# Kernel optimization log

Measured on AMD Instinct MI355X. Metric: run time of the kernel, lower is better.

Reference implementation:

```python
import jax, jax.numpy as jnp
import numpy as np

N, G, H = 500_000, 25_000, 256


def setup_inputs() -> dict:
    key = jax.random.key(0)
    ks = jax.random.split(key, 8)
    node = jax.random.normal(ks[0], (N, H), dtype=jnp.float32)
    super_node = jax.random.normal(ks[1], (G, H), dtype=jnp.float32)
    segment_ids = jnp.sort(jax.random.randint(ks[2], (N,), 0, G, dtype=jnp.int32))
    s = 0.05
    return {
        "node": node,
        "super_node": super_node,
        "segment_ids": segment_ids,
        "w_align": jax.random.normal(ks[3], (2 * H, 1), jnp.float32) * s,
        "b_align": jnp.zeros((1,), jnp.float32),
        "w_attend": jax.random.normal(ks[4], (H, H), jnp.float32) * s,
        "b_attend": jnp.zeros((H,), jnp.float32),
        "w_ih": jax.random.normal(ks[5], (H, 3 * H), jnp.float32) * s,
        "w_hh": jax.random.normal(ks[6], (H, 3 * H), jnp.float32) * s,
        "b_ih": jnp.zeros((3 * H,), jnp.float32),
        "b_hh": jnp.zeros((3 * H,), jnp.float32),
    }


def reference(node, super_node, segment_ids, w_align, b_align, w_attend,
              b_attend, w_ih, w_hh, b_ih, b_hh):
    g = super_node.shape[0]
    h = node.shape[1]
    # super_node = F.leaky_relu(super_node)
    s = jax.nn.leaky_relu(super_node)  # slope 0.01 (torch default)
    # cal_alignment(cat([node, broadcast_nodes(super)])) == node@Wn + (s@Ws)[seg]
    wn, ws = w_align[:h], w_align[h:]
    score = jax.nn.leaky_relu(node @ wn + (s @ ws)[segment_ids] + b_align)  # [N,1]
    # softmax_nodes: segment-wise stable softmax
    m = jax.ops.segment_max(score, segment_ids, num_segments=g)
    w = jnp.exp(score - m[segment_ids])
    denom = jax.ops.segment_sum(w, segment_ids, num_segments=g)
    attn = w / denom[segment_ids]  # [N,1]
    # attend (dropout=0, eval)
    hidden = node @ w_attend + b_attend  # [N,H]
    # sum_nodes weighted by attention, then ELU
    ctx = jax.nn.elu(jax.ops.segment_sum(attn * hidden, segment_ids, num_segments=g))  # [G,H]
    # GRUCell(ctx, s) per torch semantics
    gi = ctx @ w_ih + b_ih
    gh = s @ w_hh + b_hh
    ir, iz, inn = jnp.split(gi, 3, axis=-1)
    hr, hz, hn = jnp.split(gh, 3, axis=-1)
    r = jax.nn.sigmoid(ir + hr)
    z = jax.nn.sigmoid(iz + hz)
    n = jnp.tanh(inn + r * hn)
    new_h = (1.0 - z) * n + z * s
    return jax.nn.relu(new_h), attn
```

## Files before the change

### kernel.cpp

```cpp
#include <hip/hip_runtime.h>
#include <math.h>

#define N_NODES 500000
#define G_SEG   25000
#define H_DIM   256
#define SPB     4

typedef __attribute__((ext_vector_type(4))) float f32x4;
typedef __attribute__((ext_vector_type(8))) short bf16x8;

__device__ __forceinline__ float leaky(float x){ return x > 0.f ? x : 0.01f * x; }

__device__ __forceinline__ ushort f2bf(float f){
  unsigned u = __float_as_uint(f);
  u += 0x7FFFu + ((u >> 16) & 1u);
  return (ushort)(u >> 16);
}

__global__ __launch_bounds__(256) void kPrep(
    const float* __restrict__ sn, const float* __restrict__ w_align,
    const int* __restrict__ seg, const float* __restrict__ w_att,
    const float* __restrict__ w_ih, const float* __restrict__ w_hh,
    float* __restrict__ s_buf, float* __restrict__ sws,
    int* __restrict__ starts, ushort* __restrict__ Bp,
    ushort* __restrict__ Bp6)
{
  int b = blockIdx.x, t = threadIdx.x;

  {
    float v = sn[b * H_DIM + t];
    float sv = leaky(v);
    s_buf[b * H_DIM + t] = sv;
    float p = sv * w_align[H_DIM + t];
    #pragma unroll
    for (int d = 1; d < 64; d <<= 1) p += __shfl_xor(p, d);
    __shared__ float red[4];
    int wid = t >> 6, lane = t & 63;
    if (lane == 0) red[wid] = p;
    __syncthreads();
    if (t == 0) sws[b] = red[0] + red[1] + red[2] + red[3];
  }

  if (b < 1954) {
    int i = b * 256 + t;
    if (i < N_NODES) {
      int s = seg[i];
      int prev = (i == 0) ? -1 : seg[i - 1];
      for (int g = prev + 1; g <= s; g++) starts[g] = i;
      if (i == N_NODES - 1)
        for (int g = s + 1; g <= G_SEG; g++) starts[g] = N_NODES;
    }
  }
  else if (b >= 2000 && b < 2256) {
    int kk = b - 2000;
    Bp[(((kk >> 3) << 8) + t) * 8 + (kk & 7)] = f2bf(w_att[kk * H_DIM + t]);
  }
  else if (b >= 2256 && b < 2768) {
    int kk = b - 2256;
    #pragma unroll
    for (int gate = 0; gate < 4; gate++) {
      float v;
      if (gate == 0)      v = (kk < 256) ? w_ih[kk * 768 + t]        : w_hh[(kk - 256) * 768 + t];
      else if (gate == 1) v = (kk < 256) ? w_ih[kk * 768 + 256 + t]  : w_hh[(kk - 256) * 768 + 256 + t];
      else if (gate == 2) v = (kk < 256) ? w_ih[kk * 768 + 512 + t]  : 0.f;
      else                v = (kk < 256) ? 0.f                       : w_hh[(kk - 256) * 768 + 512 + t];
      int n = (gate << 8) + t;
      Bp6[(((kk >> 3) << 10) + n) * 8 + (kk & 7)] = f2bf(v);
    }
  }
}

__global__ __launch_bounds__(256) void kF_score_softmax_agg(
    const float* __restrict__ node, const int* __restrict__ starts,
    const float* __restrict__ w_align, const float* __restrict__ b_align,
    const float* __restrict__ sws,
    float* __restrict__ attn_out, float* __restrict__ agg,
    float* __restrict__ bscale)
{
  __shared__ int st_s[SPB + 1];
  const int tid = threadIdx.x;
  const int g0 = blockIdx.x * SPB;
  if (tid <= SPB) st_s[tid] = starts[g0 + tid];
  __syncthreads();

  const int wv = tid >> 6, lane = tid & 63;
  const float4 wvec = ((const float4*)w_align)[lane];
  const float b0 = b_align[0];

  const int g  = g0 + wv;
  const int st = st_s[wv], en = st_s[wv + 1];
  const float swsg = sws[g];

  float m = -3.4e38f, sum = 0.f;
  f32x4 pacc = {0.f, 0.f, 0.f, 0.f};

  int r = st;
  for (; r + 3 < en; r += 4) {
    f32x4 a0 = ((const f32x4*)node)[(size_t)(r    ) * 64 + lane];
    f32x4 a1 = ((const f32x4*)node)[(size_t)(r + 1) * 64 + lane];
    f32x4 a2 = ((const f32x4*)node)[(size_t)(r + 2) * 64 + lane];
    f32x4 a3 = ((const f32x4*)node)[(size_t)(r + 3) * 64 + lane];
    float d0 = a0[0]*wvec.x + a0[1]*wvec.y + a0[2]*wvec.z + a0[3]*wvec.w;
    float d1 = a1[0]*wvec.x + a1[1]*wvec.y + a1[2]*wvec.z + a1[3]*wvec.w;
    float d2 = a2[0]*wvec.x + a2[1]*wvec.y + a2[2]*wvec.z + a2[3]*wvec.w;
    float d3 = a3[0]*wvec.x + a3[1]*wvec.y + a3[2]*wvec.z + a3[3]*wvec.w;

    float k01 = (lane & 1) ? d1 : d0;
    float s01 = (lane & 1) ? d0 : d1;
    k01 += __shfl_xor(s01, 1);
    float k23 = (lane & 1) ? d3 : d2;
    float s23 = (lane & 1) ? d2 : d3;
    k23 += __shfl_xor(s23, 1);
    float x  = (lane & 2) ? k23 : k01;
    float xs = (lane & 2) ? k01 : k23;
    x += __shfl_xor(xs, 2);
    x += __shfl_xor(x, 4);
    x += __shfl_xor(x, 8);
    x += __shfl_xor(x, 16);
    x += __shfl_xor(x, 32);

    float sc = leaky(x + swsg + b0);
    if (lane < 4) attn_out[r + lane] = sc;

    float bm = fmaxf(sc, __shfl_xor(sc, 1));
    bm = fmaxf(bm, __shfl_xor(bm, 2));
    if (bm > m) {
      float scale = __expf(m - bm);
      sum *= scale; pacc *= scale; m = bm;
    }
    float p = __expf(sc - m);
    float p0 = __shfl(p, 0);
    float p1 = __shfl(p, 1);
    float p2 = __shfl(p, 2);
    float p3 = __shfl(p, 3);
    sum += (p0 + p1) + (p2 + p3);
    pacc += p0 * a0 + p1 * a1;
    pacc += p2 * a2 + p3 * a3;
  }
  for (; r < en; r++) {
    f32x4 a = ((const f32x4*)node)[(size_t)r * 64 + lane];
    float d = a[0]*wvec.x + a[1]*wvec.y + a[2]*wvec.z + a[3]*wvec.w;
    #pragma unroll
    for (int s2 = 1; s2 < 64; s2 <<= 1) d += __shfl_xor(d, s2);
    float sc = leaky(d + swsg + b0);
    if (lane == 0) attn_out[r] = sc;
    if (sc <= m) {
      float p = __expf(sc - m);
      sum += p;
      pacc += p * a;
    } else {
      float scale = __expf(m - sc);
      sum = sum * scale + 1.f;
      pacc = pacc * scale + a;
      m = sc;
    }
  }

  float invD = (sum > 0.f) ? 1.f / sum : 0.f;
  ((f32x4*)(agg + (size_t)g * H_DIM))[lane] = pacc * invD;
  if (lane == 0) bscale[g] = (sum > 0.f) ? 1.f : 0.f;
  for (int rr = st + lane; rr < en; rr += 64)
    attn_out[rr] = __expf(attn_out[rr] - m) * invD;
}

__global__ __launch_bounds__(256, 2) void k5b_ctx(
    const float* __restrict__ agg, const ushort* __restrict__ Bp,
    const float* __restrict__ b_att, const float* __restrict__ bscale,
    float* __restrict__ ctx)
{
  __shared__ __align__(16) ushort A_lds[128 * 256];

  const int tid  = threadIdx.x;
  const int row0 = blockIdx.x * 128;

  #pragma unroll
  for (int i = 0; i < 16; i++) {
    int v = tid + i * 256;
    int r = v >> 5;
    int s = v & 31;
    int grow = row0 + r;
    f32x4 x0 = {0.f, 0.f, 0.f, 0.f}, x1 = {0.f, 0.f, 0.f, 0.f};
    if (grow < G_SEG) {
      const f32x4* p = (const f32x4*)(agg + (size_t)grow * H_DIM) + s * 2;
      x0 = p[0]; x1 = p[1];
    }
    bf16x8 t;
    t[0] = (short)f2bf(x0[0]); t[1] = (short)f2bf(x0[1]);
    t[2] = (short)f2bf(x0[2]); t[3] = (short)f2bf(x0[3]);
    t[4] = (short)f2bf(x1[0]); t[5] = (short)f2bf(x1[1]);
    t[6] = (short)f2bf(x1[2]); t[7] = (short)f2bf(x1[3]);
    *(bf16x8*)&A_lds[r * 256 + ((s ^ (r & 7)) * 8)] = t;
  }
  __syncthreads();

  const int wv  = tid >> 6;
  const int l   = tid & 63;
  const int l15 = l & 15, lq = l >> 4, l7 = l & 7;
  const int colbase = wv * 64 + l15;

  f32x4 acc[8][4];
  #pragma unroll
  for (int mf = 0; mf < 8; mf++)
    #pragma unroll
    for (int nf = 0; nf < 4; nf++)
      acc[mf][nf] = (f32x4){0.f, 0.f, 0.f, 0.f};

  for (int ks = 0; ks < 8; ks++) {
    int c = ks * 4 + lq;
    bf16x8 b[4];
    #pragma unroll
    for (int nf = 0; nf < 4; nf++)
      b[nf] = *(const bf16x8*)&Bp[(((c << 8) + colbase + nf * 16)) * 8];
    bf16x8 a[8];
    #pragma unroll
    for (int mf = 0; mf < 8; mf++)
      a[mf] = *(const bf16x8*)&A_lds[(mf * 16 + l15) * 256 + ((c ^ l7) * 8)];
    #pragma unroll
    for (int mf = 0; mf < 8; mf++)
      #pragma unroll
      for (int nf = 0; nf < 4; nf++)
        acc[mf][nf] = __builtin_amdgcn_mfma_f32_16x16x32_bf16(
            a[mf], b[nf], acc[mf][nf], 0, 0, 0);
  }

  float bias[4];
  #pragma unroll
  for (int nf = 0; nf < 4; nf++) bias[nf] = b_att[colbase + nf * 16];

  #pragma unroll
  for (int mf = 0; mf < 8; mf++) {
    #pragma unroll
    for (int r = 0; r < 4; r++) {
      int grow = row0 + mf * 16 + lq * 4 + r;
      if (grow < G_SEG) {
        float bsc = bscale[grow];
        #pragma unroll
        for (int nf = 0; nf < 4; nf++)
          ctx[(size_t)grow * H_DIM + colbase + nf * 16] =
              acc[mf][nf][r] + bias[nf] * bsc;
      }
    }
  }
}

__global__ __launch_bounds__(512, 2) void k6_mfma(
    const float* __restrict__ ctxbuf, const float* __restrict__ s_buf,
    const ushort* __restrict__ Bp6,
    const float* __restrict__ b_ih, const float* __restrict__ b_hh,
    float* __restrict__ out0)
{
  __shared__ __align__(16) ushort A_lds[64 * 512];

  const int tid  = threadIdx.x;
  const int row0 = blockIdx.x * 64;

  #pragma unroll
  for (int i = 0; i < 8; i++) {
    int v = tid + i * 512;
    int r = v >> 6;
    int s = v & 63;
    int g = row0 + r;
    f32x4 x0 = {0.f, 0.f, 0.f, 0.f}, x1 = {0.f, 0.f, 0.f, 0.f};
    if (g < G_SEG) {
      const f32x4* p = (s < 32)
          ? (const f32x4*)(ctxbuf + (size_t)g * H_DIM) + s * 2
          : (const f32x4*)(s_buf + (size_t)g * H_DIM) + (s - 32) * 2;
      x0 = p[0]; x1 = p[1];
      if (s < 32) {
        #pragma unroll
        for (int e = 0; e < 4; e++) {
          x0[e] = x0[e] > 0.f ? x0[e] : (__expf(x0[e]) - 1.f);
          x1[e] = x1[e] > 0.f ? x1[e] : (__expf(x1[e]) - 1.f);
        }
      }
    }
    bf16x8 t;
    t[0] = (short)f2bf(x0[0]); t[1] = (short)f2bf(x0[1]);
    t[2] = (short)f2bf(x0[2]); t[3] = (short)f2bf(x0[3]);
    t[4] = (short)f2bf(x1[0]); t[5] = (short)f2bf(x1[1]);
    t[6] = (short)f2bf(x1[2]); t[7] = (short)f2bf(x1[3]);
    *(bf16x8*)&A_lds[r * 512 + ((s ^ (r & 7)) * 8)] = t;
  }
  __syncthreads();

  const int wv  = tid >> 6;
  const int rh  = (wv >> 2) * 32;
  const int cw  = (wv & 3) << 6;
  const int l   = tid & 63;
  const int l15 = l & 15, lq = l >> 4, l7 = l & 7;

  f32x4 acc[4][2][4];
  #pragma unroll
  for (int gt = 0; gt < 4; gt++)
    #pragma unroll
    for (int mf = 0; mf < 2; mf++)
      #pragma unroll
      for (int nf = 0; nf < 4; nf++)
        acc[gt][mf][nf] = (f32x4){0.f, 0.f, 0.f, 0.f};

  for (int ks = 0; ks < 16; ks++) {
    int c = ks * 4 + lq;
    bf16x8 a[2];
    #pragma unroll
    for (int mf = 0; mf < 2; mf++)
      a[mf] = *(const bf16x8*)&A_lds[(rh + mf * 16 + l15) * 512 + ((c ^ l7) * 8)];
    #pragma unroll
    for (int gt = 0; gt < 4; gt++) {
      if (gt == 2 && ks >= 8) continue;
      if (gt == 3 && ks < 8) continue;
      #pragma unroll
      for (int nf = 0; nf < 4; nf++) {
        int n = (gt << 8) + cw + nf * 16 + l15;
        bf16x8 b = *(const bf16x8*)&Bp6[(((c << 10) + n)) * 8];
        acc[gt][0][nf] = __builtin_amdgcn_mfma_f32_16x16x32_bf16(
            a[0], b, acc[gt][0][nf], 0, 0, 0);
        acc[gt][1][nf] = __builtin_amdgcn_mfma_f32_16x16x32_bf16(
            a[1], b, acc[gt][1][nf], 0, 0, 0);
      }
    }
  }

  #pragma unroll
  for (int nf = 0; nf < 4; nf++) {
    int cc = cw + nf * 16 + l15;
    float bir = b_ih[cc] + b_hh[cc];
    float biz = b_ih[256 + cc] + b_hh[256 + cc];
    float bin_ = b_ih[512 + cc];
    float bhn  = b_hh[512 + cc];
    #pragma unroll
    for (int mf = 0; mf < 2; mf++) {
      #pragma unroll
      for (int rr = 0; rr < 4; rr++) {
        int grow = row0 + rh + mf * 16 + lq * 4 + rr;
        if (grow < G_SEG) {
          float v0 = acc[0][mf][nf][rr];
          float v1 = acc[1][mf][nf][rr];
          float v2 = acc[2][mf][nf][rr];
          float v3 = acc[3][mf][nf][rr];
          float r_ = 1.f / (1.f + __expf(-(v0 + bir)));
          float z_ = 1.f / (1.f + __expf(-(v1 + biz)));
          float n_ = tanhf(v2 + bin_ + r_ * (v3 + bhn));
          float sv = s_buf[(size_t)grow * H_DIM + cc];
          float nh = (1.f - z_) * n_ + z_ * sv;
          out0[(size_t)grow * H_DIM + cc] = nh > 0.f ? nh : 0.f;
        }
      }
    }
  }
}

extern "C" void kernel_launch(void* const* d_in, const int* in_sizes, int n_in,
                              void* d_out, int out_size, void* d_ws, size_t ws_size,
                              hipStream_t stream)
{
  (void)in_sizes; (void)n_in; (void)out_size; (void)ws_size;
  const float* node       = (const float*)d_in[0];
  const float* super_node = (const float*)d_in[1];
  const int*   seg        = (const int*)d_in[2];
  const float* w_align    = (const float*)d_in[3];
  const float* b_align    = (const float*)d_in[4];
  const float* w_att      = (const float*)d_in[5];
  const float* b_att      = (const float*)d_in[6];
  const float* w_ih       = (const float*)d_in[7];
  const float* w_hh       = (const float*)d_in[8];
  const float* b_ih       = (const float*)d_in[9];
  const float* b_hh       = (const float*)d_in[10];

  float* out0     = (float*)d_out;
  float* attn_out = (float*)d_out + (size_t)G_SEG * H_DIM;

  float* ws     = (float*)d_ws;
  float* s_buf  = ws;
  float* sws    = ws + 6400000;
  float* agg    = ws + 6425000;
  ushort* Bp    = (ushort*)(ws + 12825000);
  ushort* Bp6   = (ushort*)(ws + 12860000);
  float* bscale = ws + 13125000;
  int*   starts = (int*)(ws + 13150000);
  float* ctx    = ws + 13200000;

  kPrep<<<G_SEG, 256, 0, stream>>>(super_node, w_align, seg, w_att, w_ih, w_hh,
                                   s_buf, sws, starts, Bp, Bp6);
  kF_score_softmax_agg<<<G_SEG / SPB, 256, 0, stream>>>(
      node, starts, w_align, b_align, sws, attn_out, agg, bscale);
  k5b_ctx<<<(G_SEG + 127) / 128, 256, 0, stream>>>(agg, Bp, b_att, bscale, ctx);
  k6_mfma<<<(G_SEG + 63) / 64, 512, 0, stream>>>(ctx, s_buf, Bp6, b_ih, b_hh, out0);
}
```

Measured before the change: 263.4 us.

## Vectorize prep, unroll score loop by 8, emit ELU'd bf16 ctx

kPrep now handles four super-nodes per block, one wavefront each, using float4 loads and a wave-only reduction instead of an LDS reduction and barrier. The grid shrinks to G/4 blocks. The segment-softmax aggregation loop is unrolled from 4 to 8 rows per iteration to keep more node loads in flight. k5b now applies ELU and stores ctx as bf16, which halves the intermediate traffic and removes the conversion work from k6. The costs are higher register pressure in the unrolled loop and bf16 rounding of ctx one step earlier, which matches what k6 already did.

```diff
diff --git a/kernel.cpp b/kernel.cpp
--- a/kernel.cpp
+++ b/kernel.cpp
@@ -26,19 +26,19 @@
     ushort* __restrict__ Bp6)
 {
   int b = blockIdx.x, t = threadIdx.x;
+  int wv = t >> 6, lane = t & 63;
 
   {
-    float v = sn[b * H_DIM + t];
-    float sv = leaky(v);
-    s_buf[b * H_DIM + t] = sv;
-    float p = sv * w_align[H_DIM + t];
+    int g = b * 4 + wv;
+    f32x4 sv = ((const f32x4*)(sn + (size_t)g * H_DIM))[lane];
+    f32x4 wa = ((const f32x4*)(w_align + H_DIM))[lane];
+    #pragma unroll
+    for (int e = 0; e < 4; e++) sv[e] = leaky(sv[e]);
+    ((f32x4*)(s_buf + (size_t)g * H_DIM))[lane] = sv;
+    float p = sv[0]*wa[0] + sv[1]*wa[1] + sv[2]*wa[2] + sv[3]*wa[3];
     #pragma unroll
     for (int d = 1; d < 64; d <<= 1) p += __shfl_xor(p, d);
-    __shared__ float red[4];
-    int wid = t >> 6, lane = t & 63;
-    if (lane == 0) red[wid] = p;
-    __syncthreads();
-    if (t == 0) sws[b] = red[0] + red[1] + red[2] + red[3];
+    if (lane == 0) sws[g] = p;
   }
 
   if (b < 1954) {
@@ -95,47 +95,62 @@
   f32x4 pacc = {0.f, 0.f, 0.f, 0.f};
 
   int r = st;
-  for (; r + 3 < en; r += 4) {
+  for (; r + 7 < en; r += 8) {
     f32x4 a0 = ((const f32x4*)node)[(size_t)(r    ) * 64 + lane];
     f32x4 a1 = ((const f32x4*)node)[(size_t)(r + 1) * 64 + lane];
     f32x4 a2 = ((const f32x4*)node)[(size_t)(r + 2) * 64 + lane];
     f32x4 a3 = ((const f32x4*)node)[(size_t)(r + 3) * 64 + lane];
+    f32x4 a4 = ((const f32x4*)node)[(size_t)(r + 4) * 64 + lane];
+    f32x4 a5 = ((const f32x4*)node)[(size_t)(r + 5) * 64 + lane];
+    f32x4 a6 = ((const f32x4*)node)[(size_t)(r + 6) * 64 + lane];
+    f32x4 a7 = ((const f32x4*)node)[(size_t)(r + 7) * 64 + lane];
     float d0 = a0[0]*wvec.x + a0[1]*wvec.y + a0[2]*wvec.z + a0[3]*wvec.w;
     float d1 = a1[0]*wvec.x + a1[1]*wvec.y + a1[2]*wvec.z + a1[3]*wvec.w;
     float d2 = a2[0]*wvec.x + a2[1]*wvec.y + a2[2]*wvec.z + a2[3]*wvec.w;
     float d3 = a3[0]*wvec.x + a3[1]*wvec.y + a3[2]*wvec.z + a3[3]*wvec.w;
-
-    float k01 = (lane & 1) ? d1 : d0;
-    float s01 = (lane & 1) ? d0 : d1;
+    float d4 = a4[0]*wvec.x + a4[1]*wvec.y + a4[2]*wvec.z + a4[3]*wvec.w;
+    float d5 = a5[0]*wvec.x + a5[1]*wvec.y + a5[2]*wvec.z + a5[3]*wvec.w;
+    float d6 = a6[0]*wvec.x + a6[1]*wvec.y + a6[2]*wvec.z + a6[3]*wvec.w;
+    float d7 = a7[0]*wvec.x + a7[1]*wvec.y + a7[2]*wvec.z + a7[3]*wvec.w;
+
+    float k01 = (lane & 1) ? d1 : d0, s01 = (lane & 1) ? d0 : d1;
     k01 += __shfl_xor(s01, 1);
-    float k23 = (lane & 1) ? d3 : d2;
-    float s23 = (lane & 1) ? d2 : d3;
+    float k23 = (lane & 1) ? d3 : d2, s23 = (lane & 1) ? d2 : d3;
     k23 += __shfl_xor(s23, 1);
-    float x  = (lane & 2) ? k23 : k01;
-    float xs = (lane & 2) ? k01 : k23;
-    x += __shfl_xor(xs, 2);
-    x += __shfl_xor(x, 4);
+    float k45 = (lane & 1) ? d5 : d4, s45 = (lane & 1) ? d4 : d5;
+    k45 += __shfl_xor(s45, 1);
+    float k67 = (lane & 1) ? d7 : d6, s67 = (lane & 1) ? d6 : d7;
+    k67 += __shfl_xor(s67, 1);
+    float xa = (lane & 2) ? k23 : k01, sa = (lane & 2) ? k01 : k23;
+    xa += __shfl_xor(sa, 2);
+    float xb = (lane & 2) ? k67 : k45, sb = (lane & 2) ? k45 : k67;
+    xb += __shfl_xor(sb, 2);
+    float x = (lane & 4) ? xb : xa, sx = (lane & 4) ? xa : xb;
+    x += __shfl_xor(sx, 4);
     x += __shfl_xor(x, 8);
     x += __shfl_xor(x, 16);
     x += __shfl_xor(x, 32);
 
     float sc = leaky(x + swsg + b0);
-    if (lane < 4) attn_out[r + lane] = sc;
+    if (lane < 8) attn_out[r + lane] = sc;
 
     float bm = fmaxf(sc, __shfl_xor(sc, 1));
     bm = fmaxf(bm, __shfl_xor(bm, 2));
+    bm = fmaxf(bm, __shfl_xor(bm, 4));
     if (bm > m) {
       float scale = __expf(m - bm);
       sum *= scale; pacc *= scale; m = bm;
     }
     float p = __expf(sc - m);
-    float p0 = __shfl(p, 0);
-    float p1 = __shfl(p, 1);
-    float p2 = __shfl(p, 2);
-    float p3 = __shfl(p, 3);
-    sum += (p0 + p1) + (p2 + p3);
+    float p0 = __shfl(p, 0), p1 = __shfl(p, 1);
+    float p2 = __shfl(p, 2), p3 = __shfl(p, 3);
+    float p4 = __shfl(p, 4), p5 = __shfl(p, 5);
+    float p6 = __shfl(p, 6), p7 = __shfl(p, 7);
+    sum += ((p0 + p1) + (p2 + p3)) + ((p4 + p5) + (p6 + p7));
     pacc += p0 * a0 + p1 * a1;
     pacc += p2 * a2 + p3 * a3;
+    pacc += p4 * a4 + p5 * a5;
+    pacc += p6 * a6 + p7 * a7;
   }
   for (; r < en; r++) {
     f32x4 a = ((const f32x4*)node)[(size_t)r * 64 + lane];
@@ -166,7 +181,7 @@
 __global__ __launch_bounds__(256, 2) void k5b_ctx(
     const float* __restrict__ agg, const ushort* __restrict__ Bp,
     const float* __restrict__ b_att, const float* __restrict__ bscale,
-    float* __restrict__ ctx)
+    ushort* __restrict__ ctx_bf16)
 {
   __shared__ __align__(16) ushort A_lds[128 * 256];
 
@@ -235,16 +250,18 @@
       if (grow < G_SEG) {
         float bsc = bscale[grow];
         #pragma unroll
-        for (int nf = 0; nf < 4; nf++)
-          ctx[(size_t)grow * H_DIM + colbase + nf * 16] =
-              acc[mf][nf][r] + bias[nf] * bsc;
+        for (int nf = 0; nf < 4; nf++) {
+          float val = acc[mf][nf][r] + bias[nf] * bsc;
+          val = val > 0.f ? val : (__expf(val) - 1.f);
+          ctx_bf16[(size_t)grow * H_DIM + colbase + nf * 16] = f2bf(val);
+        }
       }
     }
   }
 }
 
 __global__ __launch_bounds__(512, 2) void k6_mfma(
-    const float* __restrict__ ctxbuf, const float* __restrict__ s_buf,
+    const ushort* __restrict__ ctx_bf16, const float* __restrict__ s_buf,
     const ushort* __restrict__ Bp6,
     const float* __restrict__ b_ih, const float* __restrict__ b_hh,
     float* __restrict__ out0)
@@ -260,25 +277,19 @@
     int r = v >> 6;
     int s = v & 63;
     int g = row0 + r;
-    f32x4 x0 = {0.f, 0.f, 0.f, 0.f}, x1 = {0.f, 0.f, 0.f, 0.f};
+    bf16x8 t = {0,0,0,0,0,0,0,0};
     if (g < G_SEG) {
-      const f32x4* p = (s < 32)
-          ? (const f32x4*)(ctxbuf + (size_t)g * H_DIM) + s * 2
-          : (const f32x4*)(s_buf + (size_t)g * H_DIM) + (s - 32) * 2;
-      x0 = p[0]; x1 = p[1];
       if (s < 32) {
-        #pragma unroll
-        for (int e = 0; e < 4; e++) {
-          x0[e] = x0[e] > 0.f ? x0[e] : (__expf(x0[e]) - 1.f);
-          x1[e] = x1[e] > 0.f ? x1[e] : (__expf(x1[e]) - 1.f);
-        }
+        t = ((const bf16x8*)(ctx_bf16 + (size_t)g * H_DIM))[s];
+      } else {
+        const f32x4* p = (const f32x4*)(s_buf + (size_t)g * H_DIM) + (s - 32) * 2;
+        f32x4 y0 = p[0], y1 = p[1];
+        t[0] = (short)f2bf(y0[0]); t[1] = (short)f2bf(y0[1]);
+        t[2] = (short)f2bf(y0[2]); t[3] = (short)f2bf(y0[3]);
+        t[4] = (short)f2bf(y1[0]); t[5] = (short)f2bf(y1[1]);
+        t[6] = (short)f2bf(y1[2]); t[7] = (short)f2bf(y1[3]);
       }
     }
-    bf16x8 t;
-    t[0] = (short)f2bf(x0[0]); t[1] = (short)f2bf(x0[1]);
-    t[2] = (short)f2bf(x0[2]); t[3] = (short)f2bf(x0[3]);
-    t[4] = (short)f2bf(x1[0]); t[5] = (short)f2bf(x1[1]);
-    t[6] = (short)f2bf(x1[2]); t[7] = (short)f2bf(x1[3]);
     *(bf16x8*)&A_lds[r * 512 + ((s ^ (r & 7)) * 8)] = t;
   }
   __syncthreads();
@@ -377,12 +388,12 @@
   ushort* Bp6   = (ushort*)(ws + 12860000);
   float* bscale = ws + 13125000;
   int*   starts = (int*)(ws + 13150000);
-  float* ctx    = ws + 13200000;
-
-  kPrep<<<G_SEG, 256, 0, stream>>>(super_node, w_align, seg, w_att, w_ih, w_hh,
-                                   s_buf, sws, starts, Bp, Bp6);
+  ushort* ctx_bf16 = (ushort*)(ws + 13200000);
+
+  kPrep<<<G_SEG / 4, 256, 0, stream>>>(super_node, w_align, seg, w_att, w_ih, w_hh,
+                                       s_buf, sws, starts, Bp, Bp6);
   kF_score_softmax_agg<<<G_SEG / SPB, 256, 0, stream>>>(
       node, starts, w_align, b_align, sws, attn_out, agg, bscale);
-  k5b_ctx<<<(G_SEG + 127) / 128, 256, 0, stream>>>(agg, Bp, b_att, bscale, ctx);
-  k6_mfma<<<(G_SEG + 63) / 64, 512, 0, stream>>>(ctx, s_buf, Bp6, b_ih, b_hh, out0);
-}
+  k5b_ctx<<<(G_SEG + 127) / 128, 256, 0, stream>>>(agg, Bp, b_att, bscale, ctx_bf16);
+  k6_mfma<<<(G_SEG + 63) / 64, 512, 0, stream>>>(ctx_bf16, s_buf, Bp6, b_ih, b_hh, out0);
+}
```

Result: no change. 258.3 us (-1.9%).
